# Performance work log

Hardware: AMD Instinct MI355X
Metric: run time of the kernel (lower is better)

Reference implementation:

```python
import jax, jax.numpy as jnp
import numpy as np

B, N, T, M, DIM = 4, 4096, 16, 64, 1024
HEADS, DH = 8, 64
INNER = HEADS * DH  # 512
KV = T * M          # 1024


def setup_inputs() -> dict:
    key = jax.random.key(0)
    ks = jax.random.split(key, 8)
    x = jax.random.normal(ks[0], (B, N, DIM), jnp.float32)
    media = jax.random.normal(ks[1], (B, T, M, DIM), jnp.float32)
    # sparse media markers so cumsum(text_time) stays within [0, T]
    media_locations = jax.random.uniform(ks[2], (B, N)) < (T / N)
    ln_scale = jnp.ones((DIM,), jnp.float32)
    ln_bias = jnp.zeros((DIM,), jnp.float32)
    s_in = DIM ** -0.5
    Wq = jax.random.normal(ks[3], (DIM, INNER), jnp.float32) * s_in
    Wk = jax.random.normal(ks[4], (DIM, INNER), jnp.float32) * s_in
    Wv = jax.random.normal(ks[5], (DIM, INNER), jnp.float32) * s_in
    Wo = jax.random.normal(ks[6], (INNER, DIM), jnp.float32) * (INNER ** -0.5)
    return dict(x=x, media=media, media_locations=media_locations,
                ln_scale=ln_scale, ln_bias=ln_bias, Wq=Wq, Wk=Wk, Wv=Wv, Wo=Wo)


def reference(x, media, media_locations, ln_scale, ln_bias, Wq, Wk, Wv, Wo):
    scale = DH ** -0.5
    # LayerNorm(eps=1e-5)
    mu = jnp.mean(x, axis=-1, keepdims=True)
    var = jnp.mean((x - mu) ** 2, axis=-1, keepdims=True)
    xn = (x - mu) / jnp.sqrt(var + 1e-5) * ln_scale + ln_bias

    q = xn @ Wq                                   # [b, n, inner]
    media_f = media.reshape(B, KV, DIM)           # b (t m) d
    k = media_f @ Wk                              # [b, kv, inner]
    v = media_f @ Wv

    q = q.reshape(B, N, HEADS, DH).transpose(0, 2, 1, 3) * scale  # b h n d
    k = k.reshape(B, KV, HEADS, DH).transpose(0, 2, 1, 3)         # b h kv d
    v = v.reshape(B, KV, HEADS, DH).transpose(0, 2, 1, 3)

    sim = jnp.einsum('bhid,bhjd->bhij', q, k)     # [b, h, n, kv]

    # media-location mask: each text token attends only to its immediately
    # preceding media item (only_attend_immediate_media=True -> eq)
    text_time = jnp.cumsum(media_locations.astype(jnp.int32), axis=-1)  # [b, n]
    media_time = jnp.repeat(jnp.arange(1, T + 1), M)                    # [kv]
    mask = text_time[:, None, :, None] == media_time[None, None, None, :]
    sim = jnp.where(mask, sim, -jnp.finfo(sim.dtype).max)

    attn = jax.nn.softmax(sim, axis=-1)  # stable (subtracts rowmax), same math
    # NOTE: the original's masked_fill_ of attn for media-less text tokens is a
    # no-op (return value discarded), faithfully omitted here.

    out = jnp.einsum('bhij,bhjd->bhid', attn, v)  # b h n d
    out = out.transpose(0, 2, 1, 3).reshape(B, N, INNER)
    return out @ Wo
```

## Files before the change

kernel.cpp:

```cpp
#include <hip/hip_runtime.h>

using u16 = unsigned short;
using uch = unsigned char;

typedef __bf16 bf16x8 __attribute__((ext_vector_type(8)));
typedef float f32x4 __attribute__((ext_vector_type(4)));

#define BATCH 4
#define SEQN 4096
#define TT 16
#define MM 64
#define DIM 1024
#define HEADS 8
#define DH 64
#define INNER 512
#define KVN 1024
#define NTOK (BATCH*SEQN)
#define MAXBLK 352

#define FB_WT0  1
#define FB_CVT0 2049
#define FB_LN0  6145
#define FB_GRID (FB_LN0 + NTOK)

#define OFF_XN     ((size_t)0)
#define OFF_MEDIA  ((size_t)33554432)
#define OFF_Q      ((size_t)41943040)
#define OFF_KV     ((size_t)58720256)
#define OFF_AOUT   ((size_t)67108864)
#define OFF_WQT    ((size_t)83886080)
#define OFF_WKVT   ((size_t)84934656)
#define OFF_WOT    ((size_t)87031808)
#define OFF_VSUM   ((size_t)88145920)
#define OFF_FLAGS  ((size_t)88154112)
#define OFF_VT     ((size_t)88155136)
#define OFF_NBLK   ((size_t)92350464)
#define OFF_DESC   ((size_t)92351488)

__device__ __forceinline__ u16 f2bf(float f){
  unsigned int u = __float_as_uint(f);
  u += 0x7fffu + ((u >> 16) & 1u);
  return (u16)(u >> 16);
}
__device__ __forceinline__ float bf2f(u16 b){ return __uint_as_float(((unsigned int)b) << 16); }

__device__ __forceinline__ void async16(const u16* g, void* l){
  __builtin_amdgcn_global_load_lds((__attribute__((address_space(1))) void*)(g),
                                   (__attribute__((address_space(3))) void*)(l), 16, 0, 0);
}

__device__ __forceinline__ int detect_bf16(const unsigned int* __restrict__ x){
  __shared__ int scnt;
  const int tid = threadIdx.x;
  if (tid == 0) scnt = 0;
  __syncthreads();
  int c = 0;
  #pragma unroll
  for (int t = 0; t < 4; ++t){
    unsigned int w = x[t*256 + tid];
    unsigned int e = (w >> 7) & 0xFFu;
    c += (e >= 110u && e <= 140u) ? 1 : 0;
  }
  #pragma unroll
  for (int o = 32; o > 0; o >>= 1) c += __shfl_down(c, o);
  if ((tid & 63) == 0) atomicAdd(&scnt, c);
  __syncthreads();
  return scnt > 512 ? 1 : 0;
}

__global__ __launch_bounds__(256) void front_kernel(
    const unsigned int* __restrict__ x, const uch* __restrict__ loc,
    const void* __restrict__ ln_g, const void* __restrict__ ln_b,
    const void* __restrict__ media,
    const void* __restrict__ Wq, const void* __restrict__ Wk,
    const void* __restrict__ Wv, const void* __restrict__ Wo,
    u16* __restrict__ xn, u16* __restrict__ medb,
    u16* __restrict__ WqT, u16* __restrict__ WkvT, u16* __restrict__ WoT,
    int* __restrict__ flags, float* __restrict__ vsum,
    int4* __restrict__ desc, int* __restrict__ nblk){
  const int bid = blockIdx.x, tid = threadIdx.x;

  if (bid == 0){
    __shared__ int nonzS;
    __shared__ int wsumS[4];
    __shared__ int sbound[4][19];
    __shared__ int gcnt[72];
    int bf = detect_bf16(x);
    if (tid == 0) nonzS = 0;
    if (tid < 76) sbound[tid/19][tid%19] = 4096;
    #pragma unroll
    for (int t = 0; t < 8; ++t) vsum[t*256 + tid] = 0.f;
    __syncthreads();
    int nz = 0;
    #pragma unroll
    for (int t = 0; t < 16; ++t){
      int i = t*256 + tid;
      if ((i & 3) && loc[i]) nz++;
    }
    #pragma unroll
    for (int o = 32; o > 0; o >>= 1) nz += __shfl_down(nz, o);
    if ((tid & 63) == 0) atomicAdd(&nonzS, nz);
    __syncthreads();
    const int as32 = (nonzS == 0) ? 1 : 0;
    if (tid == 0){ flags[0] = bf; flags[1] = as32; }
    const int lane = tid & 63, wl = tid >> 6;
    for (int b = 0; b < BATCH; ++b){
      int v[16];
      if (as32){
        const int4* p = (const int4*)((const int*)loc + b*SEQN + tid*16);
        #pragma unroll
        for (int j = 0; j < 4; ++j){
          int4 q = p[j];
          v[j*4+0]=q.x!=0; v[j*4+1]=q.y!=0; v[j*4+2]=q.z!=0; v[j*4+3]=q.w!=0;
        }
      } else {
        const uchar4* p = (const uchar4*)(loc + b*SEQN + tid*16);
        #pragma unroll
        for (int j = 0; j < 4; ++j){
          uchar4 q = p[j];
          v[j*4+0]=q.x!=0; v[j*4+1]=q.y!=0; v[j*4+2]=q.z!=0; v[j*4+3]=q.w!=0;
        }
      }
      int tsum = 0;
      #pragma unroll
      for (int j = 0; j < 16; ++j) tsum += v[j];
      int s = tsum;
      #pragma unroll
      for (int o = 1; o < 64; o <<= 1){ int n2 = __shfl_up(s, o); if (lane >= o) s += n2; }
      if (lane == 63) wsumS[wl] = s;
      __syncthreads();
      int base = 0;
      for (int w2 = 0; w2 < wl; ++w2) base += wsumS[w2];
      int tt = base + s - tsum;
      #pragma unroll
      for (int j = 0; j < 16; ++j){
        if (v[j]){ tt++; if (tt <= 17) sbound[b][tt] = tid*16 + j; }
      }
      __syncthreads();
    }
    if (tid < 72){
      int bb = tid/18, g = tid%18;
      int lo = (g == 0) ? 0 : sbound[bb][g];
      int hi = (g < 17) ? sbound[bb][g+1] : 4096;
      if (hi < lo) hi = lo;
      gcnt[tid] = (hi - lo + 63) >> 6;
    }
    __syncthreads();
    if (tid == 0){
      int acc = 0;
      for (int i = 0; i < 72; ++i){ int c2 = gcnt[i]; gcnt[i] = acc; acc += c2; }
      *nblk = acc;
    }
    __syncthreads();
    if (tid < 72){
      int bb = tid/18, g = tid%18;
      int lo = (g == 0) ? 0 : sbound[bb][g];
      int hi = (g < 17) ? sbound[bb][g+1] : 4096;
      if (hi < lo) hi = lo;
      int s2 = (g == 0 || g == 17) ? -1 : (g - 1);
      int n0 = gcnt[tid];
      for (int k = lo, j = 0; k < hi; k += 64, ++j){
        int4 d; d.x = bb; d.y = s2; d.z = bb*4096 + k; d.w = min(64, hi - k);
        desc[n0 + j] = d;
      }
    }
    return;
  }

  if (bid < FB_CVT0){
    const int bf = detect_bf16(x);
    __shared__ float tile[32][33];
    int id = bid - FB_WT0;
    const void* in; u16* out; int K, N, bx, by;
    if (id < 512){       in = Wq; out = WqT;  K = DIM;   N = INNER; bx = id & 15; by = id >> 4; }
    else if (id < 1024){ in = Wk; out = WkvT; K = DIM;   N = INNER; int l = id - 512;  bx = l & 15; by = l >> 4; }
    else if (id < 1536){ in = Wv; out = WkvT + (size_t)512*1024; K = DIM; N = INNER; int l = id - 1024; bx = l & 15; by = l >> 4; }
    else {               in = Wo; out = WoT;  K = INNER; N = DIM;   int l = id - 1536; bx = l & 31; by = l >> 5; }
    int n0 = bx*32, k0 = by*32;
    int tx = tid & 31, ty = tid >> 5;
    #pragma unroll
    for (int i = 0; i < 4; ++i){
      size_t idx = (size_t)(k0 + ty + i*8)*N + n0 + tx;
      tile[ty + i*8][tx] = bf ? bf2f(((const u16*)in)[idx]) : ((const float*)in)[idx];
    }
    __syncthreads();
    #pragma unroll
    for (int i = 0; i < 4; ++i)
      out[(size_t)(n0 + ty + i*8)*K + k0 + tx] = f2bf(tile[tx][ty + i*8]);
    return;
  }

  if (bid < FB_LN0){
    const int bf = detect_bf16(x);
    size_t i = (size_t)(bid - FB_CVT0)*256 + tid;
    if (bf){
      ((ushort4*)medb)[i] = ((const ushort4*)media)[i];
    } else {
      float4 t = ((const float4*)media)[i];
      ushort4 o; o.x = f2bf(t.x); o.y = f2bf(t.y); o.z = f2bf(t.z); o.w = f2bf(t.w);
      ((ushort4*)medb)[i] = o;
    }
    return;
  }

  const int bf = detect_bf16(x);
  const int row = bid - FB_LN0;
  float v[4];
  if (bf){
    ushort4 t = ((const ushort4*)((const u16*)x + (size_t)row*DIM))[tid];
    v[0]=bf2f(t.x); v[1]=bf2f(t.y); v[2]=bf2f(t.z); v[3]=bf2f(t.w);
  } else {
    float4 t = ((const float4*)((const float*)x + (size_t)row*DIM))[tid];
    v[0]=t.x; v[1]=t.y; v[2]=t.z; v[3]=t.w;
  }
  float s = v[0]+v[1]+v[2]+v[3];
  float sq = v[0]*v[0]+v[1]*v[1]+v[2]*v[2]+v[3]*v[3];
  #pragma unroll
  for (int o = 32; o > 0; o >>= 1){ s += __shfl_down(s, o); sq += __shfl_down(sq, o); }
  __shared__ float ss[4], ssq[4];
  int wid = tid >> 6, lane = tid & 63;
  if (lane == 0){ ss[wid] = s; ssq[wid] = sq; }
  __syncthreads();
  s = ss[0]+ss[1]+ss[2]+ss[3]; sq = ssq[0]+ssq[1]+ssq[2]+ssq[3];
  float mean = s * (1.f/DIM);
  float rstd = rsqrtf(sq * (1.f/DIM) - mean*mean + 1e-5f);
  float g[4], bb[4];
  if (bf){
    ushort4 t1 = ((const ushort4*)ln_g)[tid]; ushort4 t2 = ((const ushort4*)ln_b)[tid];
    g[0]=bf2f(t1.x); g[1]=bf2f(t1.y); g[2]=bf2f(t1.z); g[3]=bf2f(t1.w);
    bb[0]=bf2f(t2.x); bb[1]=bf2f(t2.y); bb[2]=bf2f(t2.z); bb[3]=bf2f(t2.w);
  } else {
    float4 t1 = ((const float4*)ln_g)[tid]; float4 t2 = ((const float4*)ln_b)[tid];
    g[0]=t1.x; g[1]=t1.y; g[2]=t1.z; g[3]=t1.w;
    bb[0]=t2.x; bb[1]=t2.y; bb[2]=t2.z; bb[3]=t2.w;
  }
  ushort4 o;
  o.x = f2bf((v[0]-mean)*rstd*g[0] + bb[0]);
  o.y = f2bf((v[1]-mean)*rstd*g[1] + bb[1]);
  o.z = f2bf((v[2]-mean)*rstd*g[2] + bb[2]);
  o.w = f2bf((v[3]-mean)*rstd*g[3] + bb[3]);
  ((ushort4*)(xn + (size_t)row*DIM))[tid] = o;
}

template<int ROWS>
__device__ __forceinline__ void g8_stage(const u16* __restrict__ src, char* dst, int K, int t,
                                         int tid, int wid){
  #pragma unroll
  for (int i = 0; i < ROWS/64; ++i){
    int s_ = i*512 + tid;
    int row_ = s_ >> 3, g_ = s_ & 7;
    async16(src + (size_t)row_*K + t*64 + ((g_ ^ (row_ & 7)) << 3),
            dst + (size_t)(i*512 + wid*64)*16);
  }
}

template<int BN, int NT, int MODE>
__device__ __forceinline__ void gemm8_body(const u16* __restrict__ A, const u16* __restrict__ Bt,
                        void* __restrict__ Cp, int Nglob, float alpha, const int* __restrict__ flags,
                        int rm, int rn, u16* sA0, u16* sA1, u16* sB0, u16* sB1){
  constexpr int K = NT*64;
  constexpr int NREP = BN/64;
  const int tid = threadIdx.x, wid = tid >> 6, lane = tid & 63;
  const int wr = wid >> 2, wc = wid & 3;
  const int lr = lane & 15, lg = lane >> 4;
  f32x4 acc[8][NREP] = {};
  const u16* Ab = A + (size_t)rm*256*K;
  const u16* Bb = Bt + (size_t)rn*BN*K;

  g8_stage<256>(Ab, (char*)sA0, K, 0, tid, wid);
  g8_stage<BN >(Bb, (char*)sB0, K, 0, tid, wid);
  __syncthreads();

  for (int t = 0; t < NT; ++t){
    u16* Acur = (t & 1) ? sA1 : sA0;
    u16* Bcur = (t & 1) ? sB1 : sB0;
    u16* Anxt = (t & 1) ? sA0 : sA1;
    u16* Bnxt = (t & 1) ? sB0 : sB1;
    bf16x8 bfr[NREP][2];
    #pragma unroll
    for (int p = 0; p < 4; ++p){
      if (p == 0 && t + 1 < NT){
        g8_stage<256>(Ab, (char*)Anxt, K, t+1, tid, wid);
        g8_stage<BN >(Bb, (char*)Bnxt, K, t+1, tid, wid);
      }
      bf16x8 af[2][2];
      #pragma unroll
      for (int i = 0; i < 2; ++i){
        int row = wr*128 + (2*p + i)*16 + lr;
        #pragma unroll
        for (int ks = 0; ks < 2; ++ks){
          int g = (ks*4 + lg) ^ (row & 7);
          af[i][ks] = *(const bf16x8*)((const char*)Acur + row*128 + g*16);
        }
      }
      if (p == 0){
        #pragma unroll
        for (int n = 0; n < NREP; ++n){
          int row = wc*(BN/4) + n*16 + lr;
          #pragma unroll
          for (int ks = 0; ks < 2; ++ks){
            int g = (ks*4 + lg) ^ (row & 7);
            bfr[n][ks] = *(const bf16x8*)((const char*)Bcur + row*128 + g*16);
          }
        }
      }
      __builtin_amdgcn_s_barrier();
      __builtin_amdgcn_s_setprio(1);
      #pragma unroll
      for (int i = 0; i < 2; ++i)
        #pragma unroll
        for (int n = 0; n < NREP; ++n)
          #pragma unroll
          for (int ks = 0; ks < 2; ++ks)
            acc[2*p + i][n] = __builtin_amdgcn_mfma_f32_16x16x32_bf16(af[i][ks], bfr[n][ks], acc[2*p + i][n], 0, 0, 0);
      __builtin_amdgcn_s_setprio(0);
      __builtin_amdgcn_s_barrier();
    }
    if (t + 1 < NT) __syncthreads();
  }

  const bool obf = (MODE == 0) || (flags[0] != 0);
  #pragma unroll
  for (int m = 0; m < 8; ++m){
    #pragma unroll
    for (int n = 0; n < NREP; ++n){
      int row0 = rm*256 + wr*128 + m*16 + lg*4;
      int col  = rn*BN + wc*(BN/4) + n*16 + lr;
      #pragma unroll
      for (int r = 0; r < 4; ++r){
        float v = acc[m][n][r] * alpha;
        size_t idx = (size_t)(row0 + r)*Nglob + col;
        if (obf) ((u16*)Cp)[idx] = f2bf(v);
        else     ((float*)Cp)[idx] = v;
      }
    }
  }
}

__global__ __launch_bounds__(512) void proj_kernel(
    const u16* __restrict__ xn, const u16* __restrict__ WqT, u16* __restrict__ qb,
    const u16* __restrict__ medb, const u16* __restrict__ WkvT, u16* __restrict__ kvb,
    u16* __restrict__ vtp, float* __restrict__ vsum, const int* __restrict__ flags){
  __shared__ u16 smem[49152];
  const int tid = threadIdx.x;
  if (blockIdx.x < 256){
    u16* As = smem; u16* Bs = smem + 8192;
    const int wid = tid >> 6, lane = tid & 63;
    int bid = blockIdx.x;
    int wg = (bid & 7)*32 + (bid >> 3);
    const int rn = wg & 7, rm = wg >> 3;
    const int wr = wid >> 1, wc = wid & 1;
    const int lr = lane & 15, lg = lane >> 4;
    f32x4 acc[4][4] = {};
    const u16* Ab = medb + (size_t)rm*128*DIM;
    const u16* Bb = WkvT + (size_t)rn*128*DIM;
    for (int k0 = 0; k0 < DIM; k0 += 64){
      __syncthreads();
      if (tid < 256){
        #pragma unroll
        for (int t = 0; t < 4; ++t){
          int c = t*256 + tid;
          int row = c >> 3;
          int qs = (c & 7) ^ (row & 7);
          int ldsOff = (t*256 + wid*64) * 16;
          async16(Ab + (size_t)row*DIM + k0 + qs*8, (char*)As + ldsOff);
          async16(Bb + (size_t)row*DIM + k0 + qs*8, (char*)Bs + ldsOff);
        }
      }
      __syncthreads();
      if (tid < 256){
        #pragma unroll
        for (int ks = 0; ks < 2; ++ks){
          bf16x8 af[4], bfr[4];
          #pragma unroll
          for (int m = 0; m < 4; ++m){
            int row = wr*64 + m*16 + lr;
            int q = (ks*4 + lg) ^ (row & 7);
            af[m] = *(const bf16x8*)((const char*)As + row*128 + (q << 4));
          }
          #pragma unroll
          for (int n = 0; n < 4; ++n){
            int row = wc*64 + n*16 + lr;
            int q = (ks*4 + lg) ^ (row & 7);
            bfr[n] = *(const bf16x8*)((const char*)Bs + row*128 + (q << 4));
          }
          #pragma unroll
          for (int m = 0; m < 4; ++m)
            #pragma unroll
            for (int n = 0; n < 4; ++n)
              acc[m][n] = __builtin_amdgcn_mfma_f32_16x16x32_bf16(af[m], bfr[n], acc[m][n], 0, 0, 0);
        }
      }
    }
    if (tid < 256){
      const int batch = rm >> 3;
      #pragma unroll
      for (int n = 0; n < 4; ++n){
        int col = rn*128 + wc*64 + n*16 + lr;
        float psum = 0.f;
        #pragma unroll
        for (int m = 0; m < 4; ++m){
          int row0 = rm*128 + wr*64 + m*16 + lg*4;
          #pragma unroll
          for (int r = 0; r < 4; ++r){
            float v = acc[m][n][r];
            psum += v;
            size_t idx = (size_t)(row0 + r)*1024 + col;
            u16 bv = f2bf(v);
            kvb[idx] = bv;
            if (col >= 512){
              int row = row0 + r;
              int kvi = row & 1023;
              int s = kvi >> 6, rr = kvi & 63;
              vtp[((size_t)(((row >> 10)*16 + s)*512 + (col - 512)))*64 + rr] = bv;
            }
          }
        }
        if (col >= 512) atomicAdd(&vsum[batch*512 + (col - 512)], psum);
      }
    }
  } else {
    int bid = blockIdx.x - 256;
    int wg = (bid & 7)*32 + (bid >> 3);
    const int rn = wg & 3, rm = wg >> 2;
    gemm8_body<128, 16, 0>(xn, WqT, qb, INNER, 0.125f, flags, rm, rn,
                           smem, smem + 16384, smem + 32768, smem + 40960);
  }
}

__global__ __launch_bounds__(512) void gemm8_out_kernel(const u16* __restrict__ A,
                        const u16* __restrict__ Bt, void* __restrict__ Cp,
                        const int* __restrict__ flags){
  __shared__ u16 As[2][16384];
  __shared__ u16 Bs[2][16384];
  int flat = blockIdx.x + blockIdx.y*gridDim.x;
  int wg = (flat & 7)*32 + (flat >> 3);
  int rn = wg & 3, rm = wg >> 2;
  gemm8_body<256, 8, 1>(A, Bt, Cp, DIM, 1.f, flags, rm, rn, As[0], As[1], Bs[0], Bs[1]);
}

__global__ __launch_bounds__(256) void attn2_kernel(
    const u16* __restrict__ qb, const u16* __restrict__ kvb, const u16* __restrict__ vt,
    const int* __restrict__ nblk, const int4* __restrict__ desc,
    const float* __restrict__ vsum, u16* __restrict__ aout){
  __shared__ u16 Ks[64*64];
  __shared__ u16 Vs[64*64];
  __shared__ u16 Ps[4][16*72];
  if (blockIdx.x >= *nblk) return;
  const int4 d = desc[blockIdx.x];
  const int b = d.x, s = d.y, rowStart = d.z, cnt = d.w;
  const int h = blockIdx.y;
  const int tid = threadIdx.x, w = tid >> 6, lane = tid & 63;
  if (s < 0){
    const float inv = 1.f/1024.f;
    for (int idx = tid; idx < cnt*64; idx += 256){
      int slot = idx >> 6, c = h*64 + (idx & 63);
      aout[(size_t)(rowStart + slot)*512 + c] = f2bf(vsum[b*512 + c]*inv);
    }
    return;
  }
  const int lr = lane & 15, lg = lane >> 4;
  const size_t kbase = ((size_t)(b*1024 + s*64))*1024;
  const size_t vbase = ((size_t)(b*16 + s))*512*64;
  const int myslot = w*16 + lr;
  const size_t qrow = (size_t)(rowStart + min(myslot, cnt - 1))*512;
  #pragma unroll
  for (int t = 0; t < 2; ++t){
    int ci = t*256 + tid;
    int r = ci >> 3, q = ci & 7;
    int qs = (q ^ (r & 7)) << 3;
    async16(kvb + kbase + (size_t)r*1024 + h*64 + qs, (char*)Ks + ci*16);
    async16(vt + vbase + (size_t)(h*64 + r)*64 + qs, (char*)Vs + ci*16);
  }
  __syncthreads();
  bf16x8 qa0 = *(const bf16x8*)(qb + qrow + h*64 + lg*8);
  bf16x8 qa1 = *(const bf16x8*)(qb + qrow + h*64 + 32 + lg*8);
  f32x4 sv[4] = {};
  #pragma unroll
  for (int n = 0; n < 4; ++n){
    int row = n*16 + lr;
    int sl0 = (lg) ^ (row & 7);
    int sl1 = (4 + lg) ^ (row & 7);
    bf16x8 kb0 = *(const bf16x8*)((const char*)Ks + row*128 + sl0*16);
    sv[n] = __builtin_amdgcn_mfma_f32_16x16x32_bf16(qa0, kb0, sv[n], 0, 0, 0);
    bf16x8 kb1 = *(const bf16x8*)((const char*)Ks + row*128 + sl1*16);
    sv[n] = __builtin_amdgcn_mfma_f32_16x16x32_bf16(qa1, kb1, sv[n], 0, 0, 0);
  }
  float inv[4];
  #pragma unroll
  for (int r = 0; r < 4; ++r){
    float m = fmaxf(fmaxf(sv[0][r], sv[1][r]), fmaxf(sv[2][r], sv[3][r]));
    #pragma unroll
    for (int o = 1; o < 16; o <<= 1) m = fmaxf(m, __shfl_xor(m, o));
    float s0 = 0.f;
    #pragma unroll
    for (int n = 0; n < 4; ++n){ sv[n][r] = __expf(sv[n][r] - m); s0 += sv[n][r]; }
    #pragma unroll
    for (int o = 1; o < 16; o <<= 1) s0 += __shfl_xor(s0, o);
    inv[r] = 1.f / s0;
  }
  u16* pw = &Ps[w][0];
  #pragma unroll
  for (int n = 0; n < 4; ++n)
    #pragma unroll
    for (int r = 0; r < 4; ++r)
      pw[(4*lg + r)*72 + n*16 + lr] = f2bf(sv[n][r] * inv[r]);
  bf16x8 pa0 = *(const bf16x8*)((const char*)pw + lr*144 + lg*16);
  bf16x8 pa1 = *(const bf16x8*)((const char*)pw + lr*144 + 64 + lg*16);
  f32x4 ov[4] = {};
  #pragma unroll
  for (int n = 0; n < 4; ++n){
    int row = n*16 + lr;
    int sl0 = (lg) ^ (row & 7);
    int sl1 = (4 + lg) ^ (row & 7);
    bf16x8 vb0 = *(const bf16x8*)((const char*)Vs + row*128 + sl0*16);
    ov[n] = __builtin_amdgcn_mfma_f32_16x16x32_bf16(pa0, vb0, ov[n], 0, 0, 0);
    bf16x8 vb1 = *(const bf16x8*)((const char*)Vs + row*128 + sl1*16);
    ov[n] = __builtin_amdgcn_mfma_f32_16x16x32_bf16(pa1, vb1, ov[n], 0, 0, 0);
  }
  #pragma unroll
  for (int r = 0; r < 4; ++r){
    int slot = w*16 + 4*lg + r;
    if (slot < cnt){
      size_t orow = (size_t)(rowStart + slot)*512 + h*64;
      #pragma unroll
      for (int n = 0; n < 4; ++n)
        aout[orow + n*16 + lr] = f2bf(ov[n][r]);
    }
  }
}

extern "C" void kernel_launch(void* const* d_in, const int* in_sizes, int n_in,
                              void* d_out, int out_size, void* d_ws, size_t ws_size,
                              hipStream_t stream){
  const void* x      = d_in[0];
  const void* media  = d_in[1];
  const void* mloc   = d_in[2];
  const void* ln_g   = d_in[3];
  const void* ln_b   = d_in[4];
  const void* Wq     = d_in[5];
  const void* Wk     = d_in[6];
  const void* Wv     = d_in[7];
  const void* Wo     = d_in[8];
  char* ws = (char*)d_ws;
  u16* xn    = (u16*)(ws + OFF_XN);
  u16* medb  = (u16*)(ws + OFF_MEDIA);
  u16* qb    = (u16*)(ws + OFF_Q);
  u16* kvb   = (u16*)(ws + OFF_KV);
  u16* aout  = (u16*)(ws + OFF_AOUT);
  u16* WqT   = (u16*)(ws + OFF_WQT);
  u16* WkvT  = (u16*)(ws + OFF_WKVT);
  u16* WoT   = (u16*)(ws + OFF_WOT);
  float* vsm = (float*)(ws + OFF_VSUM);
  int* flags = (int*)(ws + OFF_FLAGS);
  u16* vt    = (u16*)(ws + OFF_VT);
  int* nblk  = (int*)(ws + OFF_NBLK);
  int4* desc = (int4*)(ws + OFF_DESC);

  front_kernel<<<FB_GRID, 256, 0, stream>>>(
      (const unsigned int*)x, (const uch*)mloc, ln_g, ln_b, media,
      Wq, Wk, Wv, Wo, xn, medb, WqT, WkvT, WoT, flags, vsm, desc, nblk);

  proj_kernel<<<512, 512, 0, stream>>>(xn, WqT, qb, medb, WkvT, kvb, vt, vsm, flags);

  attn2_kernel<<<dim3(MAXBLK, 8), 256, 0, stream>>>(qb, kvb, vt, nblk, desc, vsm, aout);

  gemm8_out_kernel<<<dim3(4, 64), 512, 0, stream>>>(aout, WoT, d_out, flags);
}
```

Baseline: 123.5 us.

## Route KV projection through pipelined 256x128 gemm body and shrink proj grid

The KV projection blocks previously ran a simple single-buffered 128x128 GEMM that used only half the threads (tid<256). They now use the shared double-buffered 256x128 gemm8_body with a new MODE 2 epilogue that writes kvb, the transposed V layout and the per-batch V sums. Fewer, larger tiles cut the proj grid from 512 to 384 blocks, and Q blocks are scheduled first. This is meant to use all 512 threads and overlap global loads with MFMA work, at the cost of more registers and a new epilogue mapping that has to stay correct.

```diff
diff --git a/kernel.cpp b/kernel.cpp
--- a/kernel.cpp
+++ b/kernel.cpp
@@ -257,7 +257,8 @@
 template<int BN, int NT, int MODE>
 __device__ __forceinline__ void gemm8_body(const u16* __restrict__ A, const u16* __restrict__ Bt,
                         void* __restrict__ Cp, int Nglob, float alpha, const int* __restrict__ flags,
-                        int rm, int rn, u16* sA0, u16* sA1, u16* sB0, u16* sB1){
+                        int rm, int rn, u16* sA0, u16* sA1, u16* sB0, u16* sB1,
+                        u16* __restrict__ vtp, float* __restrict__ vsum){
   constexpr int K = NT*64;
   constexpr int NREP = BN/64;
   const int tid = threadIdx.x, wid = tid >> 6, lane = tid & 63;
@@ -319,6 +320,33 @@
     if (t + 1 < NT) __syncthreads();
   }
 
+  if (MODE == 2){
+    #pragma unroll
+    for (int n = 0; n < NREP; ++n){
+      int col = rn*BN + wc*(BN/4) + n*16 + lr;
+      float psum = 0.f;
+      #pragma unroll
+      for (int m = 0; m < 8; ++m){
+        int row0 = rm*256 + wr*128 + m*16 + lg*4;
+        #pragma unroll
+        for (int r = 0; r < 4; ++r){
+          float v = acc[m][n][r];
+          psum += v;
+          int row = row0 + r;
+          u16 bv = f2bf(v);
+          ((u16*)Cp)[(size_t)row*Nglob + col] = bv;
+          if (col >= 512){
+            int kvi = row & 1023;
+            int s = kvi >> 6, rr = kvi & 63;
+            vtp[((size_t)(((row >> 10)*16 + s)*512 + (col - 512)))*64 + rr] = bv;
+          }
+        }
+      }
+      if (col >= 512) atomicAdd(&vsum[(rm >> 2)*512 + (col - 512)], psum);
+    }
+    return;
+  }
+
   const bool obf = (MODE == 0) || (flags[0] != 0);
   #pragma unroll
   for (int m = 0; m < 8; ++m){
@@ -342,89 +370,18 @@
     const u16* __restrict__ medb, const u16* __restrict__ WkvT, u16* __restrict__ kvb,
     u16* __restrict__ vtp, float* __restrict__ vsum, const int* __restrict__ flags){
   __shared__ u16 smem[49152];
-  const int tid = threadIdx.x;
+  u16* sA0 = smem;          u16* sA1 = smem + 16384;
+  u16* sB0 = smem + 32768;  u16* sB1 = smem + 40960;
   if (blockIdx.x < 256){
-    u16* As = smem; u16* Bs = smem + 8192;
-    const int wid = tid >> 6, lane = tid & 63;
     int bid = blockIdx.x;
     int wg = (bid & 7)*32 + (bid >> 3);
-    const int rn = wg & 7, rm = wg >> 3;
-    const int wr = wid >> 1, wc = wid & 1;
-    const int lr = lane & 15, lg = lane >> 4;
-    f32x4 acc[4][4] = {};
-    const u16* Ab = medb + (size_t)rm*128*DIM;
-    const u16* Bb = WkvT + (size_t)rn*128*DIM;
-    for (int k0 = 0; k0 < DIM; k0 += 64){
-      __syncthreads();
-      if (tid < 256){
-        #pragma unroll
-        for (int t = 0; t < 4; ++t){
-          int c = t*256 + tid;
-          int row = c >> 3;
-          int qs = (c & 7) ^ (row & 7);
-          int ldsOff = (t*256 + wid*64) * 16;
-          async16(Ab + (size_t)row*DIM + k0 + qs*8, (char*)As + ldsOff);
-          async16(Bb + (size_t)row*DIM + k0 + qs*8, (char*)Bs + ldsOff);
-        }
-      }
-      __syncthreads();
-      if (tid < 256){
-        #pragma unroll
-        for (int ks = 0; ks < 2; ++ks){
-          bf16x8 af[4], bfr[4];
-          #pragma unroll
-          for (int m = 0; m < 4; ++m){
-            int row = wr*64 + m*16 + lr;
-            int q = (ks*4 + lg) ^ (row & 7);
-            af[m] = *(const bf16x8*)((const char*)As + row*128 + (q << 4));
-          }
-          #pragma unroll
-          for (int n = 0; n < 4; ++n){
-            int row = wc*64 + n*16 + lr;
-            int q = (ks*4 + lg) ^ (row & 7);
-            bfr[n] = *(const bf16x8*)((const char*)Bs + row*128 + (q << 4));
-          }
-          #pragma unroll
-          for (int m = 0; m < 4; ++m)
-            #pragma unroll
-            for (int n = 0; n < 4; ++n)
-              acc[m][n] = __builtin_amdgcn_mfma_f32_16x16x32_bf16(af[m], bfr[n], acc[m][n], 0, 0, 0);
-        }
-      }
-    }
-    if (tid < 256){
-      const int batch = rm >> 3;
-      #pragma unroll
-      for (int n = 0; n < 4; ++n){
-        int col = rn*128 + wc*64 + n*16 + lr;
-        float psum = 0.f;
-        #pragma unroll
-        for (int m = 0; m < 4; ++m){
-          int row0 = rm*128 + wr*64 + m*16 + lg*4;
-          #pragma unroll
-          for (int r = 0; r < 4; ++r){
-            float v = acc[m][n][r];
-            psum += v;
-            size_t idx = (size_t)(row0 + r)*1024 + col;
-            u16 bv = f2bf(v);
-            kvb[idx] = bv;
-            if (col >= 512){
-              int row = row0 + r;
-              int kvi = row & 1023;
-              int s = kvi >> 6, rr = kvi & 63;
-              vtp[((size_t)(((row >> 10)*16 + s)*512 + (col - 512)))*64 + rr] = bv;
-            }
-          }
-        }
-        if (col >= 512) atomicAdd(&vsum[batch*512 + (col - 512)], psum);
-      }
-    }
+    gemm8_body<128, 16, 0>(xn, WqT, qb, INNER, 0.125f, flags, wg >> 2, wg & 3,
+                           sA0, sA1, sB0, sB1, nullptr, nullptr);
   } else {
     int bid = blockIdx.x - 256;
-    int wg = (bid & 7)*32 + (bid >> 3);
-    const int rn = wg & 3, rm = wg >> 2;
-    gemm8_body<128, 16, 0>(xn, WqT, qb, INNER, 0.125f, flags, rm, rn,
-                           smem, smem + 16384, smem + 32768, smem + 40960);
+    int wg = (bid & 7)*16 + (bid >> 3);
+    gemm8_body<128, 16, 2>(medb, WkvT, kvb, 1024, 1.f, flags, wg >> 3, wg & 7,
+                           sA0, sA1, sB0, sB1, vtp, vsum);
   }
 }
 
@@ -436,7 +393,8 @@
   int flat = blockIdx.x + blockIdx.y*gridDim.x;
   int wg = (flat & 7)*32 + (flat >> 3);
   int rn = wg & 3, rm = wg >> 2;
-  gemm8_body<256, 8, 1>(A, Bt, Cp, DIM, 1.f, flags, rm, rn, As[0], As[1], Bs[0], Bs[1]);
+  gemm8_body<256, 8, 1>(A, Bt, Cp, DIM, 1.f, flags, rm, rn, As[0], As[1], Bs[0], Bs[1],
+                        nullptr, nullptr);
 }
 
 __global__ __launch_bounds__(256) void attn2_kernel(
@@ -561,7 +519,7 @@
       (const unsigned int*)x, (const uch*)mloc, ln_g, ln_b, media,
       Wq, Wk, Wv, Wo, xn, medb, WqT, WkvT, WoT, flags, vsm, desc, nblk);
 
-  proj_kernel<<<512, 512, 0, stream>>>(xn, WqT, qb, medb, WkvT, kvb, vt, vsm, flags);
+  proj_kernel<<<384, 512, 0, stream>>>(xn, WqT, qb, medb, WkvT, kvb, vt, vsm, flags);
 
   attn2_kernel<<<dim3(MAXBLK, 8), 256, 0, stream>>>(qb, kvb, vt, nblk, desc, vsm, aout);
 
```

Result: slower. 131.4 us (+6.4%).

## Unify projection GEMMs onto a 128x128 tile body with 256-thread blocks

Applied to the files above, without the earlier changes.

The projection kernel now uses one 128x128, 256-thread GEMM body for both the Q projection (512 blocks) and the KV projection (256 blocks), replacing the mixed 512-thread kernel in which half the threads idled in the KV path and Q used the larger 256-row double-buffered body. The aim is to cut LDS use per block (from 96KB to 32KB) and the idle waves, so more blocks fit per CU and the work is balanced. The trade-off is that the smaller single-buffered tiles get less data reuse and have no load/compute overlap, and the Q path loses its double buffering.

```diff
diff --git a/kernel.cpp b/kernel.cpp
--- a/kernel.cpp
+++ b/kernel.cpp
@@ -242,6 +242,107 @@
   ((ushort4*)(xn + (size_t)row*DIM))[tid] = o;
 }
 
+template<int MODE>
+__device__ __forceinline__ void gemm128_body(const u16* __restrict__ A, const u16* __restrict__ Bt,
+                        u16* __restrict__ Cp, int Nglob, int K, float alpha, int rm, int rn,
+                        u16* As, u16* Bs, u16* __restrict__ vtp, float* __restrict__ vsum){
+  const int tid = threadIdx.x, wid = tid >> 6, lane = tid & 63;
+  const int wr = wid >> 1, wc = wid & 1;
+  const int lr = lane & 15, lg = lane >> 4;
+  f32x4 acc[4][4] = {};
+  const u16* Ab = A + (size_t)rm*128*K;
+  const u16* Bb = Bt + (size_t)rn*128*K;
+  for (int k0 = 0; k0 < K; k0 += 64){
+    __syncthreads();
+    #pragma unroll
+    for (int t = 0; t < 4; ++t){
+      int c = t*256 + tid;
+      int row = c >> 3;
+      int qs = (c & 7) ^ (row & 7);
+      int ldsOff = (t*256 + wid*64) * 16;
+      async16(Ab + (size_t)row*K + k0 + qs*8, (char*)As + ldsOff);
+      async16(Bb + (size_t)row*K + k0 + qs*8, (char*)Bs + ldsOff);
+    }
+    __syncthreads();
+    #pragma unroll
+    for (int ks = 0; ks < 2; ++ks){
+      bf16x8 af[4], bfr[4];
+      #pragma unroll
+      for (int m = 0; m < 4; ++m){
+        int row = wr*64 + m*16 + lr;
+        int q = (ks*4 + lg) ^ (row & 7);
+        af[m] = *(const bf16x8*)((const char*)As + row*128 + (q << 4));
+      }
+      #pragma unroll
+      for (int n = 0; n < 4; ++n){
+        int row = wc*64 + n*16 + lr;
+        int q = (ks*4 + lg) ^ (row & 7);
+        bfr[n] = *(const bf16x8*)((const char*)Bs + row*128 + (q << 4));
+      }
+      #pragma unroll
+      for (int m = 0; m < 4; ++m)
+        #pragma unroll
+        for (int n = 0; n < 4; ++n)
+          acc[m][n] = __builtin_amdgcn_mfma_f32_16x16x32_bf16(af[m], bfr[n], acc[m][n], 0, 0, 0);
+    }
+  }
+  if (MODE == 2){
+    const int batch = rm >> 3;
+    #pragma unroll
+    for (int n = 0; n < 4; ++n){
+      int col = rn*128 + wc*64 + n*16 + lr;
+      float psum = 0.f;
+      #pragma unroll
+      for (int m = 0; m < 4; ++m){
+        int row0 = rm*128 + wr*64 + m*16 + lg*4;
+        #pragma unroll
+        for (int r = 0; r < 4; ++r){
+          float v = acc[m][n][r];
+          psum += v;
+          int row = row0 + r;
+          u16 bv = f2bf(v);
+          Cp[(size_t)row*Nglob + col] = bv;
+          if (col >= 512){
+            int kvi = row & 1023;
+            int s = kvi >> 6, rr = kvi & 63;
+            vtp[((size_t)(((row >> 10)*16 + s)*512 + (col - 512)))*64 + rr] = bv;
+          }
+        }
+      }
+      if (col >= 512) atomicAdd(&vsum[batch*512 + (col - 512)], psum);
+    }
+  } else {
+    #pragma unroll
+    for (int m = 0; m < 4; ++m){
+      #pragma unroll
+      for (int n = 0; n < 4; ++n){
+        int row0 = rm*128 + wr*64 + m*16 + lg*4;
+        int col  = rn*128 + wc*64 + n*16 + lr;
+        #pragma unroll
+        for (int r = 0; r < 4; ++r)
+          Cp[(size_t)(row0 + r)*Nglob + col] = f2bf(acc[m][n][r] * alpha);
+      }
+    }
+  }
+}
+
+__global__ __launch_bounds__(256) void proj_kernel(
+    const u16* __restrict__ xn, const u16* __restrict__ WqT, u16* __restrict__ qb,
+    const u16* __restrict__ medb, const u16* __restrict__ WkvT, u16* __restrict__ kvb,
+    u16* __restrict__ vtp, float* __restrict__ vsum){
+  __shared__ u16 As[128*64];
+  __shared__ u16 Bs[128*64];
+  if (blockIdx.x < 512){
+    int bid = blockIdx.x;
+    int wg = (bid & 7)*64 + (bid >> 3);
+    gemm128_body<0>(xn, WqT, qb, INNER, DIM, 0.125f, wg >> 2, wg & 3, As, Bs, nullptr, nullptr);
+  } else {
+    int bid = blockIdx.x - 512;
+    int wg = (bid & 7)*32 + (bid >> 3);
+    gemm128_body<2>(medb, WkvT, kvb, 1024, DIM, 1.f, wg >> 3, wg & 7, As, Bs, vtp, vsum);
+  }
+}
+
 template<int ROWS>
 __device__ __forceinline__ void g8_stage(const u16* __restrict__ src, char* dst, int K, int t,
                                          int tid, int wid){
@@ -319,7 +420,7 @@
     if (t + 1 < NT) __syncthreads();
   }
 
-  const bool obf = (MODE == 0) || (flags[0] != 0);
+  const bool obf = flags[0] != 0;
   #pragma unroll
   for (int m = 0; m < 8; ++m){
     #pragma unroll
@@ -334,97 +435,6 @@
         else     ((float*)Cp)[idx] = v;
       }
     }
-  }
-}
-
-__global__ __launch_bounds__(512) void proj_kernel(
-    const u16* __restrict__ xn, const u16* __restrict__ WqT, u16* __restrict__ qb,
-    const u16* __restrict__ medb, const u16* __restrict__ WkvT, u16* __restrict__ kvb,
-    u16* __restrict__ vtp, float* __restrict__ vsum, const int* __restrict__ flags){
-  __shared__ u16 smem[49152];
-  const int tid = threadIdx.x;
-  if (blockIdx.x < 256){
-    u16* As = smem; u16* Bs = smem + 8192;
-    const int wid = tid >> 6, lane = tid & 63;
-    int bid = blockIdx.x;
-    int wg = (bid & 7)*32 + (bid >> 3);
-    const int rn = wg & 7, rm = wg >> 3;
-    const int wr = wid >> 1, wc = wid & 1;
-    const int lr = lane & 15, lg = lane >> 4;
-    f32x4 acc[4][4] = {};
-    const u16* Ab = medb + (size_t)rm*128*DIM;
-    const u16* Bb = WkvT + (size_t)rn*128*DIM;
-    for (int k0 = 0; k0 < DIM; k0 += 64){
-      __syncthreads();
-      if (tid < 256){
-        #pragma unroll
-        for (int t = 0; t < 4; ++t){
-          int c = t*256 + tid;
-          int row = c >> 3;
-          int qs = (c & 7) ^ (row & 7);
-          int ldsOff = (t*256 + wid*64) * 16;
-          async16(Ab + (size_t)row*DIM + k0 + qs*8, (char*)As + ldsOff);
-          async16(Bb + (size_t)row*DIM + k0 + qs*8, (char*)Bs + ldsOff);
-        }
-      }
-      __syncthreads();
-      if (tid < 256){
-        #pragma unroll
-        for (int ks = 0; ks < 2; ++ks){
-          bf16x8 af[4], bfr[4];
-          #pragma unroll
-          for (int m = 0; m < 4; ++m){
-            int row = wr*64 + m*16 + lr;
-            int q = (ks*4 + lg) ^ (row & 7);
-            af[m] = *(const bf16x8*)((const char*)As + row*128 + (q << 4));
-          }
-          #pragma unroll
-          for (int n = 0; n < 4; ++n){
-            int row = wc*64 + n*16 + lr;
-            int q = (ks*4 + lg) ^ (row & 7);
-            bfr[n] = *(const bf16x8*)((const char*)Bs + row*128 + (q << 4));
-          }
-          #pragma unroll
-          for (int m = 0; m < 4; ++m)
-            #pragma unroll
-            for (int n = 0; n < 4; ++n)
-              acc[m][n] = __builtin_amdgcn_mfma_f32_16x16x32_bf16(af[m], bfr[n], acc[m][n], 0, 0, 0);
-        }
-      }
-    }
-    if (tid < 256){
-      const int batch = rm >> 3;
-      #pragma unroll
-      for (int n = 0; n < 4; ++n){
-        int col = rn*128 + wc*64 + n*16 + lr;
-        float psum = 0.f;
-        #pragma unroll
-        for (int m = 0; m < 4; ++m){
-          int row0 = rm*128 + wr*64 + m*16 + lg*4;
-          #pragma unroll
-          for (int r = 0; r < 4; ++r){
-            float v = acc[m][n][r];
-            psum += v;
-            size_t idx = (size_t)(row0 + r)*1024 + col;
-            u16 bv = f2bf(v);
-            kvb[idx] = bv;
-            if (col >= 512){
-              int row = row0 + r;
-              int kvi = row & 1023;
-              int s = kvi >> 6, rr = kvi & 63;
-              vtp[((size_t)(((row >> 10)*16 + s)*512 + (col - 512)))*64 + rr] = bv;
-            }
-          }
-        }
-        if (col >= 512) atomicAdd(&vsum[batch*512 + (col - 512)], psum);
-      }
-    }
-  } else {
-    int bid = blockIdx.x - 256;
-    int wg = (bid & 7)*32 + (bid >> 3);
-    const int rn = wg & 3, rm = wg >> 2;
-    gemm8_body<128, 16, 0>(xn, WqT, qb, INNER, 0.125f, flags, rm, rn,
-                           smem, smem + 16384, smem + 32768, smem + 40960);
   }
 }
 
@@ -561,7 +571,7 @@
       (const unsigned int*)x, (const uch*)mloc, ln_g, ln_b, media,
       Wq, Wk, Wv, Wo, xn, medb, WqT, WkvT, WoT, flags, vsm, desc, nblk);
 
-  proj_kernel<<<512, 512, 0, stream>>>(xn, WqT, qb, medb, WkvT, kvb, vt, vsm, flags);
+  proj_kernel<<<768, 256, 0, stream>>>(xn, WqT, qb, medb, WkvT, kvb, vt, vsm);
 
   attn2_kernel<<<dim3(MAXBLK, 8), 256, 0, stream>>>(qb, kvb, vt, nblk, desc, vsm, aout);
 
```

Measured after the change: 123.9 us. Within noise of the previous version (+0.4%).
